# Kernel tuning notes

Measured on AMD Instinct MI355X. Metric: run time of the kernel, lower is better.

## Reference

```python
import jax, jax.numpy as jnp
import numpy as np

ITER_STEPS = 2


def setup_inputs() -> dict:
    key = jax.random.key(0)
    ks = jax.random.split(key, 9)
    B, N, D, E = 64, 256, 512, 10  # batch, nodes, node_dim, edge types
    node = jax.random.normal(ks[0], (B, N, D), dtype=jnp.float32)
    node_mask = jax.random.randint(ks[1], (B, N), 0, 2).astype(jnp.int32)
    adj = jax.random.randint(ks[2], (E, B, N, N), 0, 2).astype(jnp.int32)
    s = 0.02
    W_nw = jax.random.normal(ks[3], (1, D), dtype=jnp.float32) * s   # node weight fc [out=1, in=D]
    b_nw = jnp.zeros((1,), dtype=jnp.float32)
    W_self = jax.random.normal(ks[4], (D, D), dtype=jnp.float32) * s
    b_self = jnp.zeros((D,), dtype=jnp.float32)
    W_edge = jax.random.normal(ks[5], (E, D, D), dtype=jnp.float32) * s  # per-edge-type Linear (no bias)
    return {"node": node, "W_nw": W_nw, "b_nw": b_nw, "W_self": W_self,
            "b_self": b_self, "W_edge": W_edge, "node_mask": node_mask, "adj": adj}


def reference(node, W_nw, b_nw, W_self, b_self, W_edge, node_mask, adj):
    # node: [B,N,D]; node_mask: [B,N] int; adj: [E=10,B,N,N] int (binary)
    B, N, D = node.shape
    m = node_mask.astype(node.dtype)
    eye = jnp.eye(N, dtype=node.dtype)
    # dd_graph = mask outer-product with zeroed diagonal: [B,N,N]
    dd = m[:, None, :] * m[:, :, None] * (1.0 - eye)
    graphs = dd[None] * adj.astype(node.dtype)  # [E,B,N,N]
    # total neighbor count across all 10 edge types, clamped to >=1 (replace_masked_values)
    neigh = graphs.sum(axis=(0, 3))                       # [B,N]
    neigh = jnp.where(neigh >= 1.0, neigh, 1.0)
    all_weight = []
    for _ in range(ITER_STEPS):
        # (1) node relatedness gate
        w = jax.nn.sigmoid(node @ W_nw.T + b_nw)[..., 0]  # [B,N]
        all_weight.append(w)
        self_info = node @ W_self.T + b_self              # [B,N,D]
        # (2) per-edge-type projection + masked adjacency matmul, summed over edge types
        proj = jnp.einsum('bnk,edk->ebnd', node, W_edge)  # [E,B,N,D]
        masked_w = jnp.where(graphs != 0, w[None, :, None, :], 0.0)  # [E,B,N,N]
        agg = jnp.einsum('ebnm,ebmd->bnd', masked_w, proj)           # [B,N,D]
        # (3) update
        node = jax.nn.relu(self_info + agg / neigh[..., None])
    return node, jnp.stack(all_weight, axis=1)  # ([B,N,D], [B,ITER,N])
```

## Files before the change

kernel.cpp:

```cpp
#include <hip/hip_runtime.h>
#include <hip/hip_bf16.h>

#define BB 64
#define NN 256
#define DD 512
#define EE 10

typedef __bf16 bf16x8 __attribute__((ext_vector_type(8)));
typedef unsigned short ushort8v __attribute__((ext_vector_type(8)));
typedef unsigned int uint4v __attribute__((ext_vector_type(4)));
typedef unsigned int uint2v __attribute__((ext_vector_type(2)));
typedef float floatx4 __attribute__((ext_vector_type(4)));
typedef float floatx16 __attribute__((ext_vector_type(16)));

typedef __attribute__((address_space(3))) unsigned short lds_us;
typedef const __attribute__((address_space(1))) unsigned short glb_us;

__device__ __forceinline__ unsigned short f2b(float f) {
    union { float f; unsigned u; } x; x.f = f;
    unsigned r = x.u + 0x7FFFu + ((x.u >> 16) & 1u);
    return (unsigned short)(r >> 16);
}
__device__ __forceinline__ float b2f(unsigned short u) {
    union { unsigned u; float f; } x; x.u = ((unsigned)u) << 16;
    return x.f;
}
__device__ __forceinline__ unsigned pack_bf16(float a, float b) {
    union { float f; unsigned u; } xa, xb2; xa.f = a; xb2.f = b;
    return __builtin_amdgcn_perm(xa.u + 0x8000u, xb2.u + 0x8000u, 0x07060302u);
}

__global__ void k_wconv(const float* __restrict__ W_edge,
                        const float* __restrict__ W_self,
                        unsigned short* __restrict__ Wf) {
    int t = blockIdx.x * 256 + threadIdx.x;
    int lane  = t & 63;
    int kstep = (t >> 6) & 31;
    int cfg   = (t >> 11) & 15;
    int e     = t >> 15;
    int dout = cfg * 32 + (lane & 31);
    int k    = kstep * 16 + (lane >> 5) * 8;
    const float* src = (e < EE) ? (W_edge + ((size_t)e * DD + dout) * DD + k)
                                : (W_self + (size_t)dout * DD + k);
    ushort8v o;
    #pragma unroll
    for (int j = 0; j < 8; j++) o[j] = f2b(src[j]);
    *(ushort8v*)(Wf + (size_t)t * 8) = o;
}

__global__ void k_graph(const int* __restrict__ adj, const int* __restrict__ mask,
                        unsigned* __restrict__ packed, float* __restrict__ recip) {
    int b = blockIdx.x >> 8;
    int n = blockIdx.x & 255;
    int lane = threadIdx.x & 63;
    int wv   = threadIdx.x >> 6;
    int m = wv * 64 + lane;
    int ok = (mask[b * NN + n] != 0) & (mask[b * NN + m] != 0) & (m != n);
    __shared__ int cnt_s[4];
    int total = 0;
    #pragma unroll
    for (int e = 0; e < EE; e++) {
        int a = adj[(((size_t)e * BB + b) * NN + n) * NN + m];
        int bit = ok & (a != 0);
        unsigned long long bal = __ballot(bit);
        if (lane == 0) {
            unsigned* dst = packed + (((size_t)e * BB + b) * NN + n) * 8 + wv * 2;
            dst[0] = (unsigned)bal;
            dst[1] = (unsigned)(bal >> 32);
        }
        total += bit;
    }
    for (int off = 32; off; off >>= 1) total += __shfl_down(total, off);
    if (lane == 0) cnt_s[wv] = total;
    __syncthreads();
    if (threadIdx.x == 0) {
        int c = cnt_s[0] + cnt_s[1] + cnt_s[2] + cnt_s[3];
        recip[b * NN + n] = 1.0f / (float)(c < 1 ? 1 : c);
    }
}

template<int TI>
__global__ __launch_bounds__(256)
void k_gt(const float* __restrict__ xf, const unsigned short* __restrict__ xbin,
          const float* __restrict__ W_nw, const float* __restrict__ b_nw,
          float* __restrict__ w_out, unsigned short* __restrict__ wTf,
          unsigned short* __restrict__ xb0) {
    int bid = blockIdx.x;
    int b  = bid >> 4;
    int ms = bid & 15;
    __shared__ float part[16][17];
    __shared__ float wsig[16];
    int t = threadIdx.x;
    int row = t >> 4;
    int seg = t & 15;
    size_t g = ((size_t)(b * NN + ms * 16 + row)) * DD + seg * 32;
    float s = 0.f;
    if (TI == 0) {
        const floatx4* xp = (const floatx4*)(xf + g);
        const floatx4* wp = (const floatx4*)(W_nw + seg * 32);
        #pragma unroll
        for (int k = 0; k < 4; k++) {
            floatx4 a = xp[2 * k], c4 = xp[2 * k + 1];
            floatx4 wa = wp[2 * k], wc = wp[2 * k + 1];
            ushort8v u;
            #pragma unroll
            for (int j = 0; j < 4; j++) {
                s += a[j] * wa[j] + c4[j] * wc[j];
                u[j] = f2b(a[j]); u[4 + j] = f2b(c4[j]);
            }
            *(ushort8v*)(xb0 + g + k * 8) = u;
        }
    } else {
        const ushort8v* xp = (const ushort8v*)(xbin + g);
        const float* wp = W_nw + seg * 32;
        #pragma unroll
        for (int k = 0; k < 4; k++) {
            ushort8v u = xp[k];
            #pragma unroll
            for (int j = 0; j < 8; j++) s += b2f(u[j]) * wp[k * 8 + j];
        }
    }
    part[row][seg] = s;
    __syncthreads();
    if (t < 16) {
        float tot = 0.f;
        #pragma unroll
        for (int i = 0; i < 16; i++) tot += part[t][i];
        float v = 1.f / (1.f + __expf(-(tot + b_nw[0])));
        wsig[t] = v;
        w_out[(b * 2 + TI) * NN + ms * 16 + t] = v;
    }
    __syncthreads();
    #pragma unroll
    for (int c = 0; c < 4; c++) {
        int slot = t + 256 * c;
        int dd_  = slot >> 6;
        int lane = slot & 63;
        int l31 = lane & 31, hi = lane >> 5;
        size_t xrow = ((size_t)(b * NN + ms * 16 + hi * 8)) * DD + dd_ * 32 + l31;
        float wv[8];
        ushort8v o;
        #pragma unroll
        for (int j = 0; j < 8; j++) {
            float xv = (TI == 0) ? xf[xrow + (size_t)j * DD] : b2f(xbin[xrow + (size_t)j * DD]);
            o[j] = f2b(xv * wsig[hi * 8 + j]);
        }
        (void)wv;
        *(ushort8v*)(wTf + ((((size_t)b * 16 + ms) * 16 + dd_) * 64 + lane) * 8) = o;
    }
}

template<int TI>
__global__ __launch_bounds__(512, 2)
void k2_heavy(const unsigned short* __restrict__ wTf,
              const unsigned short* __restrict__ xb,
              const unsigned short* __restrict__ Wf,
              const unsigned* __restrict__ packed,
              const float* __restrict__ recip,
              const float* __restrict__ b_self,
              unsigned short* __restrict__ out_bf16,
              float* __restrict__ out_f32) {
    __shared__ __attribute__((aligned(16))) unsigned short sWT[32 * 512];
    __shared__ __attribute__((aligned(16))) unsigned short sWf[2][32 * 512];
    __shared__ __attribute__((aligned(16))) unsigned short sTf[16 * 512];

    int bid = blockIdx.x;
    int ct = bid & 1;
    int p  = (bid >> 1) & 3;
    int b  = p * 16 + ((bid >> 3) & 15);
    int h  = bid >> 7;
    int w = threadIdx.x >> 6, lane = threadIdx.x & 63;
    int l31 = lane & 31, hi = lane >> 5;
    int s1_d  = w & 1;
    int s1_nb = w >> 1;
    int n1 = s1_nb * 32 + l31;
    float rn = recip[b * NN + h * 128 + n1];
    int nh2 = w & 1;
    int dh4 = w >> 1;

    floatx16 acc2[2][2];
    #pragma unroll
    for (int i = 0; i < 2; i++)
        #pragma unroll
        for (int jj = 0; jj < 2; jj++)
            #pragma unroll
            for (int q = 0; q < 16; q++) acc2[i][jj][q] = 0.f;

    auto stage_sWT = [&](int dc) {
        #pragma unroll
        for (int it = 0; it < 4; it++) {
            int c = it * 8 + w;
            const unsigned short* g = wTf +
                ((((size_t)b * 16 + (c >> 1)) * 16 + dc * 2 + (c & 1)) * 64 + lane) * 8;
            __builtin_amdgcn_global_load_lds((glb_us*)g, (lds_us*)&sWT[c * 512], 16, 0, 0);
        }
    };
    auto stage_sWf = [&](int e, int dc, int buf) {
        #pragma unroll
        for (int it = 0; it < 4; it++) {
            int c = it * 8 + w;
            const unsigned short* g = Wf +
                ((((size_t)e * 16 + ct * 8 + (c >> 2)) * 32 + dc * 4 + (c & 3)) * 64 + lane) * 8;
            __builtin_amdgcn_global_load_lds((glb_us*)g, (lds_us*)&sWf[buf][c * 512], 16, 0, 0);
        }
    };

    stage_sWT(0);
    stage_sWf(0, 0, 0);

    bf16x8 Bg[16];

    #pragma unroll 1
    for (int s = 0; s < 88; s++) {
        int e = s >> 3, dc = s & 7, cur = s & 1;
        asm volatile("s_waitcnt vmcnt(0)" ::: "memory");
        asm volatile("s_barrier" ::: "memory");
        if (s < 87) {
            int ns = s + 1;
            stage_sWf(ns >> 3, ns & 7, cur ^ 1);
        }
        if (e < EE) {
            if (dc == 0) {
                const uint4v* pp = (const uint4v*)(packed +
                    (((size_t)e * BB + b) * NN + h * 128 + n1) * 8);
                uint4v pa = pp[0], pb = pp[1];
                unsigned pw[8] = {pa[0], pa[1], pa[2], pa[3], pb[0], pb[1], pb[2], pb[3]};
                #pragma unroll
                for (int ks = 0; ks < 16; ks++) {
                    int byi = ks * 2 + hi;
                    unsigned byte = (pw[byi >> 2] >> ((byi & 3) * 8)) & 0xFFu;
                    uint4v av;
                    #pragma unroll
                    for (int pp2 = 0; pp2 < 4; pp2++) {
                        unsigned tt = (byte >> (2 * pp2)) & 3u;
                        unsigned u = (tt | (tt << 15)) & 0x10001u;
                        av[pp2] = u * 0x3F80u;
                    }
                    Bg[ks] = __builtin_bit_cast(bf16x8, av);
                }
            }
            floatx16 acc3a, acc3b;
            #pragma unroll
            for (int q = 0; q < 16; q++) { acc3a[q] = 0.f; acc3b[q] = 0.f; }
            #pragma unroll
            for (int ks = 0; ks < 8; ks++) {
                bf16x8 afrA = __builtin_bit_cast(bf16x8,
                    *(const ushort8v*)&sWT[((2 * ks) * 2 + s1_d) * 512 + lane * 8]);
                bf16x8 afrB = __builtin_bit_cast(bf16x8,
                    *(const ushort8v*)&sWT[((2 * ks + 1) * 2 + s1_d) * 512 + lane * 8]);
                acc3a = __builtin_amdgcn_mfma_f32_32x32x16_bf16(afrA, Bg[2 * ks],     acc3a, 0, 0, 0);
                acc3b = __builtin_amdgcn_mfma_f32_32x32x16_bf16(afrB, Bg[2 * ks + 1], acc3b, 0, 0, 0);
            }
            #pragma unroll
            for (int g = 0; g < 4; g++) {
                float v0 = (acc3a[g * 4 + 0] + acc3b[g * 4 + 0]) * rn;
                float v1 = (acc3a[g * 4 + 1] + acc3b[g * 4 + 1]) * rn;
                float v2 = (acc3a[g * 4 + 2] + acc3b[g * 4 + 2]) * rn;
                float v3 = (acc3a[g * 4 + 3] + acc3b[g * 4 + 3]) * rn;
                uint2v pk;
                pk[0] = pack_bf16(v1, v0);
                pk[1] = pack_bf16(v3, v2);
                int slot = (((s1_d * 2 + (g >> 1)) * 4 + s1_nb) * 64 + (g & 1) * 32 + l31);
                *(uint2v*)&sTf[slot * 8 + 4 * hi] = pk;
            }
            asm volatile("s_waitcnt lgkmcnt(0)" ::: "memory");
            asm volatile("s_barrier" ::: "memory");
            if (s + 1 < 80) stage_sWT((s + 1) & 7);
            #pragma unroll
            for (int kk = 0; kk < 4; kk++) {
                bf16x8 bfr[2];
                #pragma unroll
                for (int cb = 0; cb < 2; cb++)
                    bfr[cb] = __builtin_bit_cast(bf16x8, *(const ushort8v*)
                        &sWf[cur][(((dh4 * 2 + cb) * 4 + kk) * 64 + lane) * 8]);
                #pragma unroll
                for (int na = 0; na < 2; na++) {
                    int nb = nh2 * 2 + na;
                    bf16x8 afr = __builtin_bit_cast(bf16x8, *(const ushort8v*)
                        &sTf[((kk * 4 + nb) * 64 + lane) * 8]);
                    #pragma unroll
                    for (int cb = 0; cb < 2; cb++)
                        acc2[na][cb] = __builtin_amdgcn_mfma_f32_32x32x16_bf16(
                            afr, bfr[cb], acc2[na][cb], 0, 0, 0);
                }
            }
        } else {
            #pragma unroll
            for (int kk = 0; kk < 4; kk++) {
                bf16x8 bfr[2];
                #pragma unroll
                for (int cb = 0; cb < 2; cb++)
                    bfr[cb] = __builtin_bit_cast(bf16x8, *(const ushort8v*)
                        &sWf[cur][(((dh4 * 2 + cb) * 4 + kk) * 64 + lane) * 8]);
                #pragma unroll
                for (int na = 0; na < 2; na++) {
                    bf16x8 afr = __builtin_bit_cast(bf16x8, *(const ushort8v*)(xb +
                        ((size_t)(b * NN + h * 128 + nh2 * 64 + na * 32 + l31)) * DD +
                        dc * 64 + kk * 16 + hi * 8));
                    #pragma unroll
                    for (int cb = 0; cb < 2; cb++)
                        acc2[na][cb] = __builtin_amdgcn_mfma_f32_32x32x16_bf16(
                            afr, bfr[cb], acc2[na][cb], 0, 0, 0);
                }
            }
        }
    }
    #pragma unroll
    for (int cb = 0; cb < 2; cb++) {
        int col = ct * 256 + dh4 * 64 + cb * 32 + l31;
        float bs = b_self[col];
        #pragma unroll
        for (int na = 0; na < 2; na++) {
            #pragma unroll
            for (int rg = 0; rg < 16; rg++) {
                int row = h * 128 + nh2 * 64 + na * 32 + (rg & 3) + 8 * (rg >> 2) + 4 * hi;
                float v = acc2[na][cb][rg] + bs;
                v = v > 0.f ? v : 0.f;
                size_t gi = ((size_t)b * NN + row) * DD + col;
                if (TI == 0) out_bf16[gi] = f2b(v);
                else         out_f32[gi] = v;
            }
        }
    }
}

extern "C" void kernel_launch(void* const* d_in, const int* in_sizes, int n_in,
                              void* d_out, int out_size, void* d_ws, size_t ws_size,
                              hipStream_t stream) {
    const float* node   = (const float*)d_in[0];
    const float* W_nw   = (const float*)d_in[1];
    const float* b_nw   = (const float*)d_in[2];
    const float* W_self = (const float*)d_in[3];
    const float* b_self = (const float*)d_in[4];
    const float* W_edge = (const float*)d_in[5];
    const int*   mask   = (const int*)d_in[6];
    const int*   adj    = (const int*)d_in[7];
    float* out = (float*)d_out;
    float* out_w = out + (size_t)BB * NN * DD;

    char* ws = (char*)d_ws;
    size_t off = 0;
    unsigned short* Wf    = (unsigned short*)(ws + off); off += (size_t)11 * DD * DD * 2;
    unsigned short* wTf   = (unsigned short*)(ws + off); off += (size_t)BB * DD * NN * 2;
    unsigned short* xb0   = (unsigned short*)(ws + off); off += (size_t)BB * NN * DD * 2;
    unsigned short* xb1   = (unsigned short*)(ws + off); off += (size_t)BB * NN * DD * 2;
    unsigned*       packed= (unsigned*)(ws + off);       off += (size_t)EE * BB * NN * 8 * 4;
    float*          recip = (float*)(ws + off);          off += (size_t)BB * NN * 4;

    k_wconv<<<dim3(1408), dim3(256), 0, stream>>>(W_edge, W_self, Wf);
    k_graph<<<dim3(16384), dim3(256), 0, stream>>>(adj, mask, packed, recip);

    k_gt<0><<<dim3(1024), dim3(256), 0, stream>>>(node, nullptr, W_nw, b_nw, out_w, wTf, xb0);
    k2_heavy<0><<<dim3(256), dim3(512), 0, stream>>>(wTf, xb0, Wf, packed, recip, b_self, xb1, nullptr);

    k_gt<1><<<dim3(1024), dim3(256), 0, stream>>>(nullptr, xb1, W_nw, b_nw, out_w, wTf, nullptr);
    k2_heavy<1><<<dim3(256), dim3(512), 0, stream>>>(wTf, xb1, Wf, packed, recip, b_self, nullptr, out);
}
```

Measured before the change: 698.2 us.

## Swap loop order to dc-outer/e-inner, keep weighted node tile in registers

The heavy kernel's 88-step loop is restructured so the feature chunk (dc) is outer and edge type (e, plus the self term) is inner. The weighted-node A-fragments are loaded from LDS into registers once per dc and reused across all edge types. The sWT restage then happens only once per dc rather than every step. Adjacency bits are now unpacked every step with a one-step register prefetch, instead of once per edge type, and the block-index mapping is changed so consecutive blocks cover different batches. The aim is fewer LDS reads and restages, in exchange for more registers (16 bf16x8) and repeated unpack ALU work.

```diff
diff --git a/kernel.cpp b/kernel.cpp
--- a/kernel.cpp
+++ b/kernel.cpp
@@ -138,14 +138,12 @@
         int lane = slot & 63;
         int l31 = lane & 31, hi = lane >> 5;
         size_t xrow = ((size_t)(b * NN + ms * 16 + hi * 8)) * DD + dd_ * 32 + l31;
-        float wv[8];
         ushort8v o;
         #pragma unroll
         for (int j = 0; j < 8; j++) {
             float xv = (TI == 0) ? xf[xrow + (size_t)j * DD] : b2f(xbin[xrow + (size_t)j * DD]);
             o[j] = f2b(xv * wsig[hi * 8 + j]);
         }
-        (void)wv;
         *(ushort8v*)(wTf + ((((size_t)b * 16 + ms) * 16 + dd_) * 64 + lane) * 8) = o;
     }
 }
@@ -165,10 +163,10 @@
     __shared__ __attribute__((aligned(16))) unsigned short sTf[16 * 512];
 
     int bid = blockIdx.x;
-    int ct = bid & 1;
-    int p  = (bid >> 1) & 3;
-    int b  = p * 16 + ((bid >> 3) & 15);
-    int h  = bid >> 7;
+    int b  = bid & 63;
+    int q  = bid >> 6;
+    int h  = q >> 1;
+    int ct = q & 1;
     int w = threadIdx.x >> 6, lane = threadIdx.x & 63;
     int l31 = lane & 31, hi = lane >> 5;
     int s1_d  = w & 1;
@@ -184,7 +182,7 @@
         #pragma unroll
         for (int jj = 0; jj < 2; jj++)
             #pragma unroll
-            for (int q = 0; q < 16; q++) acc2[i][jj][q] = 0.f;
+            for (int p = 0; p < 16; p++) acc2[i][jj][p] = 0.f;
 
     auto stage_sWT = [&](int dc) {
         #pragma unroll
@@ -204,103 +202,119 @@
             __builtin_amdgcn_global_load_lds((glb_us*)g, (lds_us*)&sWf[buf][c * 512], 16, 0, 0);
         }
     };
+    auto load_packed = [&](int e, uint4v& p0, uint4v& p1) {
+        const uint4v* pp = (const uint4v*)(packed +
+            (((size_t)e * BB + b) * NN + h * 128 + n1) * 8);
+        p0 = pp[0]; p1 = pp[1];
+    };
 
     stage_sWT(0);
     stage_sWf(0, 0, 0);
-
-    bf16x8 Bg[16];
-
+    uint4v pN0, pN1;
+    load_packed(0, pN0, pN1);
+
+    bf16x8 Awt[16];
+
+    int s = 0;
     #pragma unroll 1
-    for (int s = 0; s < 88; s++) {
-        int e = s >> 3, dc = s & 7, cur = s & 1;
-        asm volatile("s_waitcnt vmcnt(0)" ::: "memory");
-        asm volatile("s_barrier" ::: "memory");
-        if (s < 87) {
-            int ns = s + 1;
-            stage_sWf(ns >> 3, ns & 7, cur ^ 1);
-        }
-        if (e < EE) {
-            if (dc == 0) {
-                const uint4v* pp = (const uint4v*)(packed +
-                    (((size_t)e * BB + b) * NN + h * 128 + n1) * 8);
-                uint4v pa = pp[0], pb = pp[1];
-                unsigned pw[8] = {pa[0], pa[1], pa[2], pa[3], pb[0], pb[1], pb[2], pb[3]};
-                #pragma unroll
-                for (int ks = 0; ks < 16; ks++) {
-                    int byi = ks * 2 + hi;
-                    unsigned byte = (pw[byi >> 2] >> ((byi & 3) * 8)) & 0xFFu;
-                    uint4v av;
-                    #pragma unroll
-                    for (int pp2 = 0; pp2 < 4; pp2++) {
-                        unsigned tt = (byte >> (2 * pp2)) & 3u;
-                        unsigned u = (tt | (tt << 15)) & 0x10001u;
-                        av[pp2] = u * 0x3F80u;
+    for (int dc = 0; dc < 8; dc++) {
+        #pragma unroll 1
+        for (int e = 0; e <= EE; e++, s++) {
+            int cur = s & 1;
+            asm volatile("s_waitcnt vmcnt(0)" ::: "memory");
+            asm volatile("s_barrier" ::: "memory");
+            if (s < 87) {
+                int ne = (e < EE) ? e + 1 : 0;
+                int ndc = (e < EE) ? dc : dc + 1;
+                stage_sWf(ne, ndc, cur ^ 1);
+            }
+            if (e < EE) {
+                unsigned pw[8] = {pN0[0], pN0[1], pN0[2], pN0[3],
+                                  pN1[0], pN1[1], pN1[2], pN1[3]};
+                if (e < EE - 1)      load_packed(e + 1, pN0, pN1);
+                else                 load_packed(0, pN0, pN1);
+                if (e == 0) {
+                    #pragma unroll
+                    for (int ms = 0; ms < 16; ms++)
+                        Awt[ms] = __builtin_bit_cast(bf16x8,
+                            *(const ushort8v*)&sWT[(ms * 2 + s1_d) * 512 + lane * 8]);
+                }
+                floatx16 acc3a, acc3b;
+                #pragma unroll
+                for (int p = 0; p < 16; p++) { acc3a[p] = 0.f; acc3b[p] = 0.f; }
+                #pragma unroll
+                for (int kp = 0; kp < 8; kp++) {
+                    uint4v av0, av1;
+                    #pragma unroll
+                    for (int half = 0; half < 2; half++) {
+                        int ks = 2 * kp + half;
+                        int byi = ks * 2 + hi;
+                        unsigned byte = (pw[byi >> 2] >> ((byi & 3) * 8)) & 0xFFu;
+                        uint4v av;
+                        #pragma unroll
+                        for (int pp2 = 0; pp2 < 4; pp2++) {
+                            unsigned tt = (byte >> (2 * pp2)) & 3u;
+                            unsigned u = (tt | (tt << 15)) & 0x10001u;
+                            av[pp2] = u * 0x3F80u;
+                        }
+                        if (half == 0) av0 = av; else av1 = av;
                     }
-                    Bg[ks] = __builtin_bit_cast(bf16x8, av);
-                }
-            }
-            floatx16 acc3a, acc3b;
-            #pragma unroll
-            for (int q = 0; q < 16; q++) { acc3a[q] = 0.f; acc3b[q] = 0.f; }
-            #pragma unroll
-            for (int ks = 0; ks < 8; ks++) {
-                bf16x8 afrA = __builtin_bit_cast(bf16x8,
-                    *(const ushort8v*)&sWT[((2 * ks) * 2 + s1_d) * 512 + lane * 8]);
-                bf16x8 afrB = __builtin_bit_cast(bf16x8,
-                    *(const ushort8v*)&sWT[((2 * ks + 1) * 2 + s1_d) * 512 + lane * 8]);
-                acc3a = __builtin_amdgcn_mfma_f32_32x32x16_bf16(afrA, Bg[2 * ks],     acc3a, 0, 0, 0);
-                acc3b = __builtin_amdgcn_mfma_f32_32x32x16_bf16(afrB, Bg[2 * ks + 1], acc3b, 0, 0, 0);
-            }
-            #pragma unroll
-            for (int g = 0; g < 4; g++) {
-                float v0 = (acc3a[g * 4 + 0] + acc3b[g * 4 + 0]) * rn;
-                float v1 = (acc3a[g * 4 + 1] + acc3b[g * 4 + 1]) * rn;
-                float v2 = (acc3a[g * 4 + 2] + acc3b[g * 4 + 2]) * rn;
-                float v3 = (acc3a[g * 4 + 3] + acc3b[g * 4 + 3]) * rn;
-                uint2v pk;
-                pk[0] = pack_bf16(v1, v0);
-                pk[1] = pack_bf16(v3, v2);
-                int slot = (((s1_d * 2 + (g >> 1)) * 4 + s1_nb) * 64 + (g & 1) * 32 + l31);
-                *(uint2v*)&sTf[slot * 8 + 4 * hi] = pk;
-            }
-            asm volatile("s_waitcnt lgkmcnt(0)" ::: "memory");
-            asm volatile("s_barrier" ::: "memory");
-            if (s + 1 < 80) stage_sWT((s + 1) & 7);
-            #pragma unroll
-            for (int kk = 0; kk < 4; kk++) {
-                bf16x8 bfr[2];
-                #pragma unroll
-                for (int cb = 0; cb < 2; cb++)
-                    bfr[cb] = __builtin_bit_cast(bf16x8, *(const ushort8v*)
-                        &sWf[cur][(((dh4 * 2 + cb) * 4 + kk) * 64 + lane) * 8]);
-                #pragma unroll
-                for (int na = 0; na < 2; na++) {
-                    int nb = nh2 * 2 + na;
-                    bf16x8 afr = __builtin_bit_cast(bf16x8, *(const ushort8v*)
-                        &sTf[((kk * 4 + nb) * 64 + lane) * 8]);
+                    acc3a = __builtin_amdgcn_mfma_f32_32x32x16_bf16(
+                        Awt[2 * kp],     __builtin_bit_cast(bf16x8, av0), acc3a, 0, 0, 0);
+                    acc3b = __builtin_amdgcn_mfma_f32_32x32x16_bf16(
+                        Awt[2 * kp + 1], __builtin_bit_cast(bf16x8, av1), acc3b, 0, 0, 0);
+                }
+                #pragma unroll
+                for (int g = 0; g < 4; g++) {
+                    float v0 = (acc3a[g * 4 + 0] + acc3b[g * 4 + 0]) * rn;
+                    float v1 = (acc3a[g * 4 + 1] + acc3b[g * 4 + 1]) * rn;
+                    float v2 = (acc3a[g * 4 + 2] + acc3b[g * 4 + 2]) * rn;
+                    float v3 = (acc3a[g * 4 + 3] + acc3b[g * 4 + 3]) * rn;
+                    uint2v pk;
+                    pk[0] = pack_bf16(v1, v0);
+                    pk[1] = pack_bf16(v3, v2);
+                    int slot = (((s1_d * 2 + (g >> 1)) * 4 + s1_nb) * 64 + (g & 1) * 32 + l31);
+                    *(uint2v*)&sTf[slot * 8 + 4 * hi] = pk;
+                }
+                asm volatile("s_waitcnt lgkmcnt(0)" ::: "memory");
+                asm volatile("s_barrier" ::: "memory");
+                if (e == 0 && dc < 7) stage_sWT(dc + 1);
+                #pragma unroll
+                for (int kk = 0; kk < 4; kk++) {
+                    bf16x8 bfr[2];
                     #pragma unroll
                     for (int cb = 0; cb < 2; cb++)
-                        acc2[na][cb] = __builtin_amdgcn_mfma_f32_32x32x16_bf16(
-                            afr, bfr[cb], acc2[na][cb], 0, 0, 0);
-                }
-            }
-        } else {
-            #pragma unroll
-            for (int kk = 0; kk < 4; kk++) {
-                bf16x8 bfr[2];
-                #pragma unroll
-                for (int cb = 0; cb < 2; cb++)
-                    bfr[cb] = __builtin_bit_cast(bf16x8, *(const ushort8v*)
-                        &sWf[cur][(((dh4 * 2 + cb) * 4 + kk) * 64 + lane) * 8]);
-                #pragma unroll
-                for (int na = 0; na < 2; na++) {
-                    bf16x8 afr = __builtin_bit_cast(bf16x8, *(const ushort8v*)(xb +
-                        ((size_t)(b * NN + h * 128 + nh2 * 64 + na * 32 + l31)) * DD +
-                        dc * 64 + kk * 16 + hi * 8));
+                        bfr[cb] = __builtin_bit_cast(bf16x8, *(const ushort8v*)
+                            &sWf[cur][(((dh4 * 2 + cb) * 4 + kk) * 64 + lane) * 8]);
+                    #pragma unroll
+                    for (int na = 0; na < 2; na++) {
+                        int nb = nh2 * 2 + na;
+                        bf16x8 afr = __builtin_bit_cast(bf16x8, *(const ushort8v*)
+                            &sTf[((kk * 4 + nb) * 64 + lane) * 8]);
+                        #pragma unroll
+                        for (int cb = 0; cb < 2; cb++)
+                            acc2[na][cb] = __builtin_amdgcn_mfma_f32_32x32x16_bf16(
+                                afr, bfr[cb], acc2[na][cb], 0, 0, 0);
+                    }
+                }
+            } else {
+                #pragma unroll
+                for (int kk = 0; kk < 4; kk++) {
+                    bf16x8 bfr[2];
                     #pragma unroll
                     for (int cb = 0; cb < 2; cb++)
-                        acc2[na][cb] = __builtin_amdgcn_mfma_f32_32x32x16_bf16(
-                            afr, bfr[cb], acc2[na][cb], 0, 0, 0);
+                        bfr[cb] = __builtin_bit_cast(bf16x8, *(const ushort8v*)
+                            &sWf[cur][(((dh4 * 2 + cb) * 4 + kk) * 64 + lane) * 8]);
+                    #pragma unroll
+                    for (int na = 0; na < 2; na++) {
+                        bf16x8 afr = __builtin_bit_cast(bf16x8, *(const ushort8v*)(xb +
+                            ((size_t)(b * NN + h * 128 + nh2 * 64 + na * 32 + l31)) * DD +
+                            dc * 64 + kk * 16 + hi * 8));
+                        #pragma unroll
+                        for (int cb = 0; cb < 2; cb++)
+                            acc2[na][cb] = __builtin_amdgcn_mfma_f32_32x32x16_bf16(
+                                afr, bfr[cb], acc2[na][cb], 0, 0, 0);
+                    }
                 }
             }
         }
```

Measured after the change: 2.372 ms. 240% more time.
